# Performance work log

Measured on AMD Instinct MI355X. Metric: run time of the kernel, lower is better.

Reference implementation:

```python
import jax, jax.numpy as jnp
import numpy as np

B, S, H, NH, DH, F, L = 4, 2048, 512, 8, 64, 2048, 4
ALPHA = 1.0   # config.lag_time_scale_alpha
EPS = 1e-12   # BERT layer_norm_eps
MS_PER_MIN = 60.0 * 1000.0


def setup_inputs() -> dict:
    key = jax.random.key(0)
    ks = jax.random.split(key, 24)
    p = lambda k, shape: (jax.random.normal(k, shape, jnp.float32) * 0.02)
    inp = {
        "query_states": jax.random.normal(ks[0], (B, S, H), jnp.float32),
        "attention_mask": jnp.zeros((B, 1, 1, S), jnp.float32),
        "position_bias": jax.random.normal(ks[1], (1, NH, S, S), jnp.float32) * 0.02,
        "timestamp": jnp.sort(jax.random.randint(ks[2], (B, S), 0, 36_000_000, jnp.int32), axis=-1),
        # stacked per-layer parameters (L leading dim)
        "wq": p(ks[3], (L, H, H)), "bq": jnp.zeros((L, H), jnp.float32),
        "wk": p(ks[4], (L, H, H)), "bk": jnp.zeros((L, H), jnp.float32),
        "wv": p(ks[5], (L, H, H)), "bv": jnp.zeros((L, H), jnp.float32),
        "wo": p(ks[6], (L, H, H)), "bo": jnp.zeros((L, H), jnp.float32),
        "ln1_g": jnp.ones((L, H), jnp.float32), "ln1_b": jnp.zeros((L, H), jnp.float32),
        "wi": p(ks[7], (L, H, F)), "bi": jnp.zeros((L, F), jnp.float32),
        "wo2": p(ks[8], (L, F, H)), "bo2": jnp.zeros((L, H), jnp.float32),
        "ln2_g": jnp.ones((L, H), jnp.float32), "ln2_b": jnp.zeros((L, H), jnp.float32),
    }
    return inp


def _ln(x, g, b):
    m = x.mean(-1, keepdims=True)
    v = ((x - m) ** 2).mean(-1, keepdims=True)
    return (x - m) / jnp.sqrt(v + EPS) * g + b


def reference(query_states, attention_mask, position_bias, timestamp,
              wq, bq, wk, bk, wv, bv, wo, bo, ln1_g, ln1_b,
              wi, bi, wo2, bo2, ln2_g, ln2_b):
    # encoder (is_decoder=False) lag-time scale: (B,1,S,S)
    lag = (timestamp[:, None, :, None] - timestamp[:, None, None, :]).astype(jnp.float32) / MS_PER_MIN
    scale = np.sqrt(DH).astype(np.float32) - ALPHA / (jnp.clip(lag, 0.0) + 1.0) + ALPHA

    x = query_states
    for l in range(L):
        def proj(w, b):
            return (x @ w + b).reshape(B, S, NH, DH).transpose(0, 2, 1, 3)  # (B,NH,S,DH)
        q, k, v = proj(wq[l], bq[l]), proj(wk[l], bk[l]), proj(wv[l], bv[l])
        scores = jnp.einsum('bhqd,bhkd->bhqk', q, k) / scale + position_bias + attention_mask
        probs = jax.nn.softmax(scores, axis=-1)
        ctx = jnp.einsum('bhqk,bhkd->bhqd', probs, v).transpose(0, 2, 1, 3).reshape(B, S, H)
        attn = _ln(ctx @ wo[l] + bo[l] + x, ln1_g[l], ln1_b[l])
        ffn = jax.nn.gelu(attn @ wi[l] + bi[l], approximate=False) @ wo2[l] + bo2[l]
        x = _ln(ffn + attn, ln2_g[l], ln2_b[l])
    return x
```

## Files before the change

kernel.cpp:

```cpp
#include <hip/hip_runtime.h>
#include <stdint.h>

typedef unsigned short u16;
using half8   = __attribute__((ext_vector_type(8))) _Float16;
using half4v  = __attribute__((ext_vector_type(4))) _Float16;
using half2v  = __attribute__((ext_vector_type(2))) _Float16;
using float4v = __attribute__((ext_vector_type(4))) float;

#define L2E 1.4426950408889634f

__device__ inline float4v f4zero() { float4v z = {0.f, 0.f, 0.f, 0.f}; return z; }

__device__ inline u16 f2h(float f) {
  union { _Float16 h; u16 u; } v; v.h = (_Float16)f; return v.u;
}
__device__ inline float h2f(u16 u) {
  union { u16 u; _Float16 h; } v; v.u = u; return (float)v.h;
}

__device__ inline half2v cvtpk(float a, float b) {
  return __builtin_bit_cast(half2v, __builtin_amdgcn_cvt_pkrtz(a, b));
}
__device__ inline _Float16 hexp2_(_Float16 x) {
  _Float16 r;
  asm("v_exp_f16 %0, %1" : "=v"(r) : "v"(x));
  return r;
}
__device__ inline float fdot2f(half2v a, float c) {
#if __has_builtin(__builtin_amdgcn_fdot2)
  typedef __attribute__((ext_vector_type(2))) __fp16 h2r;
  return __builtin_amdgcn_fdot2(__builtin_bit_cast(h2r, a),
                                __builtin_bit_cast(h2r, 0x3C003C00u), c, false);
#else
  return c + (float)a.x + (float)a.y;
#endif
}

__device__ inline void glds16(const u16* g, u16* lds_base, int lane) {
#if __has_builtin(__builtin_amdgcn_global_load_lds)
  (void)lane;
  __builtin_amdgcn_global_load_lds((const __attribute__((address_space(1))) void*)g,
                                   (__attribute__((address_space(3))) void*)lds_base,
                                   16, 0, 0);
#else
  *(uint4*)(lds_base + (size_t)lane * 8) = *(const uint4*)g;
#endif
}

__global__ __launch_bounds__(256) void transpose_cast_kernel(
    const float* __restrict__ in, u16* __restrict__ out, int K, int N, size_t out_ls) {
  __shared__ float tile[32][33];
  const int tx = threadIdx.x & 31, ty = threadIdx.x >> 5;
  in  += (size_t)blockIdx.z * K * N;
  out += (size_t)blockIdx.z * out_ls;
  const int n  = blockIdx.x * 32 + tx;
  const int k0 = blockIdx.y * 32;
#pragma unroll
  for (int j = 0; j < 32; j += 8)
    tile[ty + j][tx] = in[(size_t)(k0 + ty + j) * N + n];
  __syncthreads();
  const int k = k0 + tx;
  const int n0 = blockIdx.x * 32;
#pragma unroll
  for (int j = 0; j < 32; j += 8)
    out[(size_t)(n0 + ty + j) * K + k] = f2h(tile[tx][ty + j]);
}

__global__ __launch_bounds__(256) void cast_kernel(const float* __restrict__ in,
                                                   u16* __restrict__ out) {
  const int i = (blockIdx.x * 256 + threadIdx.x) * 4;
  float4 t = *(const float4*)(in + i);
  ushort4 o;
  o.x = f2h(t.x); o.y = f2h(t.y); o.z = f2h(t.z); o.w = f2h(t.w);
  *(ushort4*)(out + i) = o;
}

__global__ __launch_bounds__(256) void pb_tile_kernel(const float* __restrict__ pb,
                                                      u16* __restrict__ pbT) {
  const int g  = blockIdx.x * 256 + threadIdx.x;
  const int mm = g & 15;
  const int q  = (g >> 4) & 2047;
  const int kbh = g >> 15;
  const int kb = kbh & 31, h = kbh >> 5;
  const float* src = pb + ((size_t)h * 2048 + q) * 2048 + kb * 64 + mm;
  ushort4 o;
  o.x = f2h(src[0]  * L2E);
  o.y = f2h(src[16] * L2E);
  o.z = f2h(src[32] * L2E);
  o.w = f2h(src[48] * L2E);
  *(ushort4*)(pbT + ((size_t)(h * 32 + kb) * 2048 + q) * 64 + mm * 4) = o;
}

__global__ __launch_bounds__(256) void inv_tile_kernel(const int* __restrict__ ts,
                                                       u16* __restrict__ invT) {
  const int g  = blockIdx.x * 256 + threadIdx.x;
  const int mm = g & 15;
  const int q  = (g >> 4) & 2047;
  const int kb = (g >> 15) & 31;
  const int b  = g >> 20;
  const int tq = ts[b * 2048 + q];
  ushort4 o;
  u16* op = (u16*)&o;
#pragma unroll
  for (int nb = 0; nb < 4; nb++) {
    const int k = kb * 64 + nb * 16 + mm;
    const int du = tq - ts[b * 2048 + k];
    const float u = (du > 0) ? (float)du : 0.f;
    op[nb] = f2h(fmaf(u, L2E, 86561.70245333781f) *
                 __builtin_amdgcn_rcpf(fmaf(u, 9.f, 480000.f)));
  }
  *(ushort4*)(invT + ((size_t)(b * 32 + kb) * 2048 + q) * 64 + mm * 4) = o;
}

__global__ __launch_bounds__(256) void maskts_kernel(const float* __restrict__ mask,
                                                     const int* __restrict__ ts,
                                                     float* __restrict__ maskE,
                                                     float* __restrict__ tsf) {
  const int i = blockIdx.x * 256 + threadIdx.x;
  maskE[i] = mask[i] * L2E;
  tsf[i]   = (float)ts[i];
}

template <int BM, int BN, int NN, int KK, int EPI>
__global__ __launch_bounds__(256) void gemm_kernel(
    const u16* __restrict__ A, const u16* __restrict__ Wt,
    const float* __restrict__ b0, const float* __restrict__ b1, const float* __restrict__ b2,
    const u16* __restrict__ resid,
    void* __restrict__ o0, void* __restrict__ o1, void* __restrict__ o2) {
  constexpr int FI = BM / 32;
  constexpr int FJB = BN / 32;
  constexpr int FIW = BM / 32;
  constexpr int FJW = BN / 32;
  constexpr int NT = KK / 64;
  __shared__ __align__(16) u16 smem[2 * BM * 64 + 2 * BN * 64];
  u16* As0 = smem;
  u16* Bs0 = smem + 2 * BM * 64;
  const int tid = threadIdx.x, lane = tid & 63, wv = tid >> 6;
  const int quad = lane >> 4, mm = lane & 15;
  const int m0 = blockIdx.x * BM, n0 = blockIdx.y * BN;
  const int wm = (wv >> 1) * (BM / 2), wn = (wv & 1) * (BN / 2);
  const int srow = tid >> 3, slot = tid & 7;
  const int chunk = slot ^ (srow & 7);
  const u16* Ag = A  + (size_t)(m0 + srow) * KK + chunk * 8;
  const u16* Bg = Wt + (size_t)(n0 + srow) * KK + chunk * 8;
  const int sw = mm & 7;

  float4v acc[FIW][FJW];
#pragma unroll
  for (int i = 0; i < FIW; i++)
#pragma unroll
    for (int j = 0; j < FJW; j++) acc[i][j] = f4zero();

#pragma unroll
  for (int i = 0; i < FI; i++)
    glds16(Ag + (size_t)i * 32 * KK, As0 + (size_t)(wv * 8 + i * 32) * 64, lane);
#pragma unroll
  for (int j = 0; j < FJB; j++)
    glds16(Bg + (size_t)j * 32 * KK, Bs0 + (size_t)(wv * 8 + j * 32) * 64, lane);

  int cur = 0;
#pragma unroll 2
  for (int kt = 0; kt < NT; kt++) {
    __syncthreads();

    if (kt + 1 < NT) {
      const size_t ko = (size_t)(kt + 1) * 64;
#pragma unroll
      for (int i = 0; i < FI; i++)
        glds16(Ag + (size_t)i * 32 * KK + ko,
               As0 + (size_t)(cur ^ 1) * BM * 64 + (size_t)(wv * 8 + i * 32) * 64, lane);
#pragma unroll
      for (int j = 0; j < FJB; j++)
        glds16(Bg + (size_t)j * 32 * KK + ko,
               Bs0 + (size_t)(cur ^ 1) * BN * 64 + (size_t)(wv * 8 + j * 32) * 64, lane);
    }

    const u16* Ac = As0 + (size_t)cur * BM * 64;
    const u16* Bc = Bs0 + (size_t)cur * BN * 64;
#pragma unroll
    for (int ks = 0; ks < 2; ks++) {
      half8 a[FIW], b[FJW];
#pragma unroll
      for (int i = 0; i < FIW; i++)
        a[i] = *(const half8*)(Ac + (size_t)(wm + i * 16 + mm) * 64 + (size_t)((ks * 4 + quad) ^ sw) * 8);
#pragma unroll
      for (int j = 0; j < FJW; j++)
        b[j] = *(const half8*)(Bc + (size_t)(wn + j * 16 + mm) * 64 + (size_t)((ks * 4 + quad) ^ sw) * 8);
#pragma unroll
      for (int i = 0; i < FIW; i++)
#pragma unroll
        for (int j = 0; j < FJW; j++)
          acc[i][j] = __builtin_amdgcn_mfma_f32_16x16x32_f16(a[i], b[j], acc[i][j], 0, 0, 0);
    }
    cur ^= 1;
  }

#pragma unroll
  for (int j = 0; j < FJW; j++) {
    const int gn = n0 + wn + j * 16 + mm;
    const float bias = b0[gn];
#pragma unroll
    for (int i = 0; i < FIW; i++)
#pragma unroll
      for (int r = 0; r < 4; r++) {
        const int gm = m0 + wm + i * 16 + quad * 4 + r;
        const float val = acc[i][j][r] + bias;
        const size_t idx = (size_t)gm * NN + gn;
        if (EPI == 2) {
          ((u16*)o0)[idx] = f2h(val);
        } else {
          const float z  = val * 0.70710678118654752f;
          const float az = fabsf(z);
          const float t  = __builtin_amdgcn_rcpf(1.0f + 0.3275911f * az);
          const float poly = t * (0.254829592f + t * (-0.284496736f +
                             t * (1.421413741f + t * (-1.453152027f + t * 1.061405429f))));
          const float e = __builtin_amdgcn_exp2f(-az * az * L2E);
          float erf_ = 1.0f - poly * e;
          erf_ = (z < 0.0f) ? -erf_ : erf_;
          ((u16*)o0)[idx] = f2h(val * 0.5f * (1.0f + erf_));
        }
      }
  }
  (void)b1; (void)b2; (void)o1; (void)o2; (void)resid;
}

template <int NN, int KK, int EPI>
__global__ __launch_bounds__(512) void gemm8_kernel(
    const u16* __restrict__ A, const u16* __restrict__ Wt,
    const float* __restrict__ b0, const float* __restrict__ b1, const float* __restrict__ b2,
    void* __restrict__ o0, void* __restrict__ o1, void* __restrict__ o2) {
  __shared__ __align__(16) u16 smem[256 * 64 + 128 * 64];
  u16* As = smem;
  u16* Bs = smem + 256 * 64;
  const int tid = threadIdx.x, lane = tid & 63, wv = tid >> 6;
  const int quad = lane >> 4, mm = lane & 15;
  const int m0 = blockIdx.x * 256, n0 = blockIdx.y * 128;
  const int wm = (wv >> 1) * 64, wn = (wv & 1) * 64;
  const int srow = tid >> 3, slot = tid & 7;
  const int chunk = slot ^ (srow & 7);
  const u16* Ag = A  + (size_t)(m0 + srow) * KK + chunk * 8;
  const u16* Bg = Wt + (size_t)(n0 + srow) * KK + chunk * 8;
  const int sw = mm & 7;

  float4v acc[4][4];
#pragma unroll
  for (int i = 0; i < 4; i++)
#pragma unroll
    for (int j = 0; j < 4; j++) acc[i][j] = f4zero();

  for (int kte = 0; kte < KK; kte += 64) {
#pragma unroll
    for (int p = 0; p < 4; p++)
      glds16(Ag + (size_t)(p * 64) * KK + kte, As + (size_t)(p * 64 + wv * 8) * 64, lane);
#pragma unroll
    for (int p = 0; p < 2; p++)
      glds16(Bg + (size_t)(p * 64) * KK + kte, Bs + (size_t)(p * 64 + wv * 8) * 64, lane);
    __syncthreads();

#pragma unroll
    for (int ks = 0; ks < 2; ks++) {
      half8 a[4], b[4];
#pragma unroll
      for (int i = 0; i < 4; i++)
        a[i] = *(const half8*)(As + (size_t)(wm + i * 16 + mm) * 64 + (size_t)((ks * 4 + quad) ^ sw) * 8);
#pragma unroll
      for (int j = 0; j < 4; j++)
        b[j] = *(const half8*)(Bs + (size_t)(wn + j * 16 + mm) * 64 + (size_t)((ks * 4 + quad) ^ sw) * 8);
#pragma unroll
      for (int i = 0; i < 4; i++)
#pragma unroll
        for (int j = 0; j < 4; j++)
          acc[i][j] = __builtin_amdgcn_mfma_f32_16x16x32_f16(a[i], b[j], acc[i][j], 0, 0, 0);
    }
    __syncthreads();
  }

  if constexpr (EPI == 4) {
    if (n0 >= 1024) {
      const int b_ = m0 >> 11, s_base = m0 & 2047;
      const int h0 = (n0 >> 6) & 7;
      u16* T = smem;
#pragma unroll
      for (int hp = 0; hp < 2; hp++) {
        __syncthreads();
        if ((wv >> 2) == hp) {
          const int lm = wm & 127;
#pragma unroll
          for (int j = 0; j < 4; j++) {
            const int cn = wn + j * 16 + mm;
            const float bias = b2[(n0 & 511) + cn];
#pragma unroll
            for (int i = 0; i < 4; i++)
#pragma unroll
              for (int r = 0; r < 4; r++)
                T[(lm + i * 16 + quad * 4 + r) * 130 + cn] = f2h(acc[i][j][r] + bias);
          }
        }
        __syncthreads();
        const int rr = tid >> 2, sq = tid & 3;
        const int hh = rr >> 6, dd = rr & 63;
        u16* outp = (u16*)o2 + ((size_t)((b_ * 8 + h0 + hh) * 64 + dd)) * 2048
                  + s_base + hp * 128 + sq * 32;
#pragma unroll
        for (int g = 0; g < 4; g++) {
          union { u16 u[8]; uint4 v; } pk;
#pragma unroll
          for (int e = 0; e < 8; e++) {
            const int sl = sq * 32 + g * 8 + e;
            const int tl = (sl & 64) + (((sl & 3) << 4) | ((sl & 63) >> 2));
            pk.u[e] = T[tl * 130 + rr];
          }
          *(uint4*)(outp + g * 8) = pk.v;
        }
      }
      return;
    }
#pragma unroll
    for (int j = 0; j < 4; j++) {
      const int gn = n0 + wn + j * 16 + mm;
      const int which = gn >> 9, col = gn & 511, h = (gn >> 6) & 7, d = gn & 63;
      const float* bp = (which == 0) ? b0 : b1;
      const float bias = bp[col];
      u16* dst = (which == 0) ? (u16*)o0 : (u16*)o1;
#pragma unroll
      for (int i = 0; i < 4; i++)
#pragma unroll
        for (int r = 0; r < 4; r++) {
          const int gm = m0 + wm + i * 16 + quad * 4 + r;
          const int b_ = gm >> 11, s_ = gm & 2047;
          dst[((size_t)((b_ * 8 + h) * 2048 + s_)) * 64 + d] = f2h(acc[i][j][r] + bias);
        }
    }
    return;
  }

#pragma unroll
  for (int j = 0; j < 4; j++) {
    const int gn = n0 + wn + j * 16 + mm;
    const float bias = b0[gn];
#pragma unroll
    for (int i = 0; i < 4; i++)
#pragma unroll
      for (int r = 0; r < 4; r++) {
        const int gm = m0 + wm + i * 16 + quad * 4 + r;
        const float val = acc[i][j][r] + bias;
        const size_t idx = (size_t)gm * NN + gn;
        const float z  = val * 0.70710678118654752f;
        const float az = fabsf(z);
        const float t  = __builtin_amdgcn_rcpf(1.0f + 0.3275911f * az);
        const float poly = t * (0.254829592f + t * (-0.284496736f +
                           t * (1.421413741f + t * (-1.453152027f + t * 1.061405429f))));
        const float e = __builtin_amdgcn_exp2f(-az * az * L2E);
        float erf_ = 1.0f - poly * e;
        erf_ = (z < 0.0f) ? -erf_ : erf_;
        ((u16*)o0)[idx] = f2h(val * 0.5f * (1.0f + erf_));
      }
  }
}

template <int TILED>
__global__ __launch_bounds__(512) void flash4_kernel(
    const u16* __restrict__ Q, const u16* __restrict__ Kb, const u16* __restrict__ Vt,
    const u16* __restrict__ pbT, const u16* __restrict__ invT,
    const float* __restrict__ pb32,
    const float* __restrict__ maskE, const float* __restrict__ tsf,
    u16* __restrict__ ctx) {
  __shared__ __align__(16) u16 Kls[2][64 * 64];
  __shared__ __align__(16) u16 Vls[2][64 * 64];
  __shared__ __align__(16) u16 P[8][16 * 64];
  const int tid = threadIdx.x, lane = tid & 63, w = tid >> 6;
  const int quad = lane >> 4, mm = lane & 15;
  const int bh = blockIdx.y, b_ = bh >> 3, h_ = bh & 7;
  const int q0 = blockIdx.x * 128 + w * 16;
  const size_t qk_base = (size_t)bh * 2048 * 64;
  const size_t v_base  = (size_t)bh * 64 * 2048;
  const int srow = lane >> 3, slot = lane & 7;
  const int chunk = slot ^ srow;
  const int sw = mm & 7;

  const u16* Kgl = Kb + qk_base + (size_t)(w * 8 + srow) * 64 + chunk * 8;
  const u16* Vgl = Vt + v_base + (size_t)(w * 8 + srow) * 2048 + chunk * 8;

  glds16(Kgl, &Kls[0][(w * 8) * 64], lane);
  glds16(Vgl, &Vls[0][(w * 8) * 64], lane);

  half8 aq[2];
#pragma unroll
  for (int t = 0; t < 2; t++)
    aq[t] = *(const half8*)(Q + qk_base + (size_t)(q0 + mm) * 64 + t * 32 + quad * 8);

  float tqf[4];
  if (TILED < 2) {
#pragma unroll
    for (int r = 0; r < 4; r++) tqf[r] = tsf[b_ * 2048 + q0 + quad * 4 + r];
  }

  float l_r[4] = {0.f, 0.f, 0.f, 0.f};
  float4v o[4];
#pragma unroll
  for (int ob = 0; ob < 4; ob++) o[ob] = f4zero();

  ushort4 pbc[4], invc[4]; float tkc[4], mkc[4];
  if (TILED >= 1) {
#pragma unroll
    for (int r = 0; r < 4; r++)
      pbc[r] = *(const ushort4*)(pbT + ((size_t)(h_ * 32) * 2048 + q0 + quad * 4 + r) * 64 + mm * 4);
  }
  if (TILED == 2) {
#pragma unroll
    for (int r = 0; r < 4; r++)
      invc[r] = *(const ushort4*)(invT + ((size_t)(b_ * 32) * 2048 + q0 + quad * 4 + r) * 64 + mm * 4);
  } else {
#pragma unroll
    for (int nb = 0; nb < 4; nb++) tkc[nb] = tsf[b_ * 2048 + nb * 16 + mm];
  }
#pragma unroll
  for (int nb = 0; nb < 4; nb++) mkc[nb] = maskE[b_ * 2048 + nb * 16 + mm];

  int cur = 0;
  for (int kt = 0; kt < 32; kt++) {
    const int k0 = kt * 64;
    __syncthreads();

    const int kn = (kt < 31) ? kt + 1 : kt;
    ushort4 pbn[4], invn[4]; float tkn[4], mkn[4];
    if (TILED >= 1) {
#pragma unroll
      for (int r = 0; r < 4; r++)
        pbn[r] = *(const ushort4*)(pbT + ((size_t)(h_ * 32 + kn) * 2048 + q0 + quad * 4 + r) * 64 + mm * 4);
    }
    if (TILED == 2) {
#pragma unroll
      for (int r = 0; r < 4; r++)
        invn[r] = *(const ushort4*)(invT + ((size_t)(b_ * 32 + kn) * 2048 + q0 + quad * 4 + r) * 64 + mm * 4);
    } else {
#pragma unroll
      for (int nb = 0; nb < 4; nb++) tkn[nb] = tsf[b_ * 2048 + kn * 64 + nb * 16 + mm];
    }
#pragma unroll
    for (int nb = 0; nb < 4; nb++) mkn[nb] = maskE[b_ * 2048 + kn * 64 + nb * 16 + mm];

    if (kt < 31) {
      const size_t ko = (size_t)(kt + 1) * 4096;
      const size_t vo = (size_t)(kt + 1) * 64;
      glds16(Kgl + ko, &Kls[cur ^ 1][(w * 8) * 64], lane);
      glds16(Vgl + vo, &Vls[cur ^ 1][(w * 8) * 64], lane);
    }

    const u16* Kc = Kls[cur];
    float4v s[4];
    __builtin_amdgcn_s_setprio(1);
#pragma unroll
    for (int nb = 0; nb < 4; nb++) {
      const half8 kf0 = *(const half8*)(Kc + (size_t)(nb * 16 + mm) * 64 + (size_t)(quad ^ sw) * 8);
      const half8 kf1 = *(const half8*)(Kc + (size_t)(nb * 16 + mm) * 64 + (size_t)((4 + quad) ^ sw) * 8);
      s[nb] = __builtin_amdgcn_mfma_f32_16x16x32_f16(aq[0], kf0, f4zero(), 0, 0, 0);
      s[nb] = __builtin_amdgcn_mfma_f32_16x16x32_f16(aq[1], kf1, s[nb], 0, 0, 0);
    }
    __builtin_amdgcn_s_setprio(0);

    const half2v mk01 = cvtpk(mkc[0], mkc[1]);
    const half2v mk23 = cvtpk(mkc[2], mkc[3]);
#pragma unroll
    for (int r = 0; r < 4; r++) {
      half2v pb01, pb23, iv01, iv23;
      if (TILED >= 1) {
        pb01 = *(const half2v*)&pbc[r].x;
        pb23 = *(const half2v*)&pbc[r].z;
      } else {
        float pv[4];
#pragma unroll
        for (int nb = 0; nb < 4; nb++)
          pv[nb] = pb32[((size_t)h_ * 2048 + q0 + quad * 4 + r) * 2048 + k0 + nb * 16 + mm] * L2E;
        pb01 = cvtpk(pv[0], pv[1]); pb23 = cvtpk(pv[2], pv[3]);
      }
      if (TILED == 2) {
        iv01 = *(const half2v*)&invc[r].x;
        iv23 = *(const half2v*)&invc[r].z;
      } else {
        float ivv[4];
#pragma unroll
        for (int nb = 0; nb < 4; nb++) {
          const float u = fmaxf(tqf[r] - tkc[nb], 0.f);
          ivv[nb] = fmaf(u, L2E, 86561.70245333781f) *
                    __builtin_amdgcn_rcpf(fmaf(u, 9.f, 480000.f));
        }
        iv01 = cvtpk(ivv[0], ivv[1]); iv23 = cvtpk(ivv[2], ivv[3]);
      }
      const half2v s01 = cvtpk(s[0][r], s[1][r]);
      const half2v s23 = cvtpk(s[2][r], s[3][r]);
      const half2v t01 = __builtin_elementwise_fma(s01, iv01, pb01 + mk01);
      const half2v t23 = __builtin_elementwise_fma(s23, iv23, pb23 + mk23);
      half2v p01, p23;
      p01.x = hexp2_(t01.x); p01.y = hexp2_(t01.y);
      p23.x = hexp2_(t23.x); p23.y = hexp2_(t23.y);
      l_r[r] = fdot2f(p01, l_r[r]);
      l_r[r] = fdot2f(p23, l_r[r]);
      const int prow = quad * 4 + r;
      union { half2v h2[2]; half4v h4; } uu;
      uu.h2[0] = p01; uu.h2[1] = p23;
      *(half4v*)((char*)P[w] + prow * 128 + ((mm * 8) ^ ((prow & 7) << 4))) = uu.h4;
    }

    const u16* Vc = Vls[cur];
    const char* Pb = (const char*)P[w] + mm * 128;
    const int pxor = (mm & 7) << 4;
    const half8 ap0 = *(const half8*)(Pb + ((quad * 16) ^ pxor));
    const half8 ap1 = *(const half8*)(Pb + ((64 + quad * 16) ^ pxor));
    __builtin_amdgcn_s_setprio(1);
#pragma unroll
    for (int ob = 0; ob < 4; ob++) {
      const half8 vf0 = *(const half8*)(Vc + (size_t)(ob * 16 + mm) * 64 + (size_t)(quad ^ sw) * 8);
      const half8 vf1 = *(const half8*)(Vc + (size_t)(ob * 16 + mm) * 64 + (size_t)((4 + quad) ^ sw) * 8);
      o[ob] = __builtin_amdgcn_mfma_f32_16x16x32_f16(ap0, vf0, o[ob], 0, 0, 0);
      o[ob] = __builtin_amdgcn_mfma_f32_16x16x32_f16(ap1, vf1, o[ob], 0, 0, 0);
    }
    __builtin_amdgcn_s_setprio(0);

#pragma unroll
    for (int r = 0; r < 4; r++) { pbc[r] = pbn[r]; invc[r] = invn[r]; }
#pragma unroll
    for (int nb = 0; nb < 4; nb++) { tkc[nb] = tkn[nb]; mkc[nb] = mkn[nb]; }
    cur ^= 1;
  }

#pragma unroll
  for (int r = 0; r < 4; r++) {
    float l = l_r[r];
#pragma unroll
    for (int sh = 1; sh < 16; sh <<= 1) l += __shfl_xor(l, sh, 64);
    const float rl = __builtin_amdgcn_rcpf(l);
    const int qrow = q0 + quad * 4 + r;
#pragma unroll
    for (int ob = 0; ob < 4; ob++)
      ctx[((size_t)b_ * 2048 + qrow) * 512 + h_ * 64 + ob * 16 + mm] = f2h(o[ob][r] * rl);
  }
}

__global__ __launch_bounds__(256) void ln_kernel(
    const u16* __restrict__ in, const u16* __restrict__ resid,
    const float* __restrict__ g, const float* __restrict__ bb,
    float* __restrict__ of, u16* __restrict__ obf) {
  const int lane = threadIdx.x & 63, w = threadIdx.x >> 6;
  const int row = blockIdx.x * 4 + w;
  const size_t base = (size_t)row * 512 + lane * 8;
  union { uint4 v; u16 u[8]; } a, b;
  a.v = *(const uint4*)(in + base);
  b.v = *(const uint4*)(resid + base);
  float v[8];
#pragma unroll
  for (int i = 0; i < 8; i++) v[i] = h2f(a.u[i]) + h2f(b.u[i]);
  float s = 0.f;
#pragma unroll
  for (int i = 0; i < 8; i++) s += v[i];
#pragma unroll
  for (int sh = 1; sh < 64; sh <<= 1) s += __shfl_xor(s, sh, 64);
  const float mean = s * (1.0f / 512.0f);
  float sq = 0.f;
#pragma unroll
  for (int i = 0; i < 8; i++) { const float d = v[i] - mean; sq += d * d; }
#pragma unroll
  for (int sh = 1; sh < 64; sh <<= 1) sq += __shfl_xor(sq, sh, 64);
  const float rstd = rsqrtf(sq * (1.0f / 512.0f) + 1e-12f);
#pragma unroll
  for (int i = 0; i < 8; i++) {
    const int col = lane * 8 + i;
    const float y = (v[i] - mean) * rstd * g[col] + bb[col];
    if (of) of[(size_t)row * 512 + col] = y;
    obf[(size_t)row * 512 + col] = f2h(y);
  }
}

extern "C" void kernel_launch(void* const* d_in, const int* in_sizes, int n_in,
                              void* d_out, int out_size, void* d_ws, size_t ws_size,
                              hipStream_t stream) {
  const float* x_in = (const float*)d_in[0];
  const float* mask = (const float*)d_in[1];
  const float* pb   = (const float*)d_in[2];
  const int*   ts   = (const int*)d_in[3];
  const float* wq = (const float*)d_in[4];  const float* bq = (const float*)d_in[5];
  const float* wk = (const float*)d_in[6];  const float* bk = (const float*)d_in[7];
  const float* wvp = (const float*)d_in[8]; const float* bv = (const float*)d_in[9];
  const float* wo = (const float*)d_in[10]; const float* bo = (const float*)d_in[11];
  const float* ln1g = (const float*)d_in[12]; const float* ln1b = (const float*)d_in[13];
  const float* wi = (const float*)d_in[14]; const float* bi = (const float*)d_in[15];
  const float* wo2 = (const float*)d_in[16]; const float* bo2 = (const float*)d_in[17];
  const float* ln2g = (const float*)d_in[18]; const float* ln2b = (const float*)d_in[19];

  char* ws = (char*)d_ws;
  const size_t o_wqkv  = 0;
  const size_t o_woT   = 6291456;
  const size_t o_wiT   = 8388608;
  const size_t o_wo2T  = 16777216;
  const size_t o_maskE = 25165824;
  const size_t o_tsf   = 25198592;
  const size_t o_xbf   = 25231360;
  const size_t o_qb    = 33619968;
  const size_t o_kb    = 42008576;
  const size_t o_vb    = 50397184;
  const size_t o_ctx   = 58785792;
  const size_t o_attnb = 67174400;
  const size_t o_tmp   = 75563008;
  const size_t o_pbT   = 92340224;
  const size_t o_invT  = 159449088;
  const int tiled = (ws_size >= o_invT + 33554432ull) ? 2
                  : (ws_size >= o_pbT + 67108864ull) ? 1 : 0;

  u16*   wqkvT = (u16*)(ws + o_wqkv);
  u16*   woT   = (u16*)(ws + o_woT);
  u16*   wiT   = (u16*)(ws + o_wiT);
  u16*   wo2T  = (u16*)(ws + o_wo2T);
  float* maskE = (float*)(ws + o_maskE);
  float* tsf   = (float*)(ws + o_tsf);
  u16*   xbf   = (u16*)(ws + o_xbf);
  u16*   qb    = (u16*)(ws + o_qb);
  u16*   kb    = (u16*)(ws + o_kb);
  u16*   vb    = (u16*)(ws + o_vb);
  u16*   ctx   = (u16*)(ws + o_ctx);
  u16*   hb    = (u16*)(ws + o_qb);
  u16*   attnb = (u16*)(ws + o_attnb);
  u16*   tmp16 = (u16*)(ws + o_tmp);
  u16*   pbT   = (u16*)(ws + o_pbT);
  u16*   invT  = (u16*)(ws + o_invT);

  const dim3 blk(256);
  const dim3 blk512(512);
  transpose_cast_kernel<<<dim3(16, 16, 4), blk, 0, stream>>>(wq,  wqkvT,          512, 512, 786432);
  transpose_cast_kernel<<<dim3(16, 16, 4), blk, 0, stream>>>(wk,  wqkvT + 262144, 512, 512, 786432);
  transpose_cast_kernel<<<dim3(16, 16, 4), blk, 0, stream>>>(wvp, wqkvT + 524288, 512, 512, 786432);
  transpose_cast_kernel<<<dim3(16, 16, 4), blk, 0, stream>>>(wo,  woT,  512, 512,  262144);
  transpose_cast_kernel<<<dim3(64, 16, 4), blk, 0, stream>>>(wi,  wiT,  512, 2048, 1048576);
  transpose_cast_kernel<<<dim3(16, 64, 4), blk, 0, stream>>>(wo2, wo2T, 2048, 512, 1048576);
  maskts_kernel<<<32, blk, 0, stream>>>(mask, ts, maskE, tsf);
  cast_kernel<<<4096, blk, 0, stream>>>(x_in, xbf);
  if (tiled >= 1) pb_tile_kernel<<<32768, blk, 0, stream>>>(pb, pbT);
  if (tiled == 2) inv_tile_kernel<<<16384, blk, 0, stream>>>(ts, invT);

  for (int l = 0; l < 4; l++) {
    gemm8_kernel<1536, 512, 4><<<dim3(32, 12), blk512, 0, stream>>>(
        xbf, wqkvT + (size_t)l * 786432, bq + l * 512, bk + l * 512, bv + l * 512,
        qb, kb, vb);
    if (tiled == 2)
      flash4_kernel<2><<<dim3(16, 32), blk512, 0, stream>>>(qb, kb, vb, pbT, invT, pb, maskE, tsf, ctx);
    else if (tiled == 1)
      flash4_kernel<1><<<dim3(16, 32), blk512, 0, stream>>>(qb, kb, vb, pbT, nullptr, pb, maskE, tsf, ctx);
    else
      flash4_kernel<0><<<dim3(16, 32), blk512, 0, stream>>>(qb, kb, vb, nullptr, nullptr, pb, maskE, tsf, ctx);
    gemm_kernel<128, 64, 512, 512, 2><<<dim3(64, 8), blk, 0, stream>>>(
        ctx, woT + (size_t)l * 262144, bo + l * 512, nullptr, nullptr, nullptr,
        tmp16, nullptr, nullptr);
    ln_kernel<<<2048, blk, 0, stream>>>(tmp16, xbf, ln1g + l * 512, ln1b + l * 512,
                                        nullptr, attnb);
    gemm8_kernel<2048, 512, 3><<<dim3(32, 16), blk512, 0, stream>>>(
        attnb, wiT + (size_t)l * 1048576, bi + l * 2048, nullptr, nullptr,
        hb, nullptr, nullptr);
    gemm_kernel<128, 64, 512, 2048, 2><<<dim3(64, 8), blk, 0, stream>>>(
        hb, wo2T + (size_t)l * 1048576, bo2 + l * 512, nullptr, nullptr, nullptr,
        tmp16, nullptr, nullptr);
    ln_kernel<<<2048, blk, 0, stream>>>(tmp16, attnb, ln2g + l * 512, ln2b + l * 512,
                                        (l == 3) ? (float*)d_out : nullptr, xbf);
  }
  (void)in_sizes; (void)n_in; (void)out_size;
}
```

Before: 1.125 ms.

## Split attention key range across two blocks and merge partial contexts

Adds a third grid dimension to the flash attention kernel so each block handles half of the key tiles. Each half writes a normalized fp16 partial context plus its row sum. A new combine kernel then merges the two halves, weighting each by its share of the total softmax denominator. The goal is to double the number of blocks and fill the GPU better, at the cost of extra partial-output traffic, another launch, and a second fp16 rounding step.

Result: slower. 1.161 ms (+3.2%).

```diff
diff --git a/kernel.cpp b/kernel.cpp
--- a/kernel.cpp
+++ b/kernel.cpp
@@ -364,13 +364,15 @@
     const u16* __restrict__ pbT, const u16* __restrict__ invT,
     const float* __restrict__ pb32,
     const float* __restrict__ maskE, const float* __restrict__ tsf,
-    u16* __restrict__ ctx) {
+    u16* __restrict__ ctxPart, float* __restrict__ lPart) {
   __shared__ __align__(16) u16 Kls[2][64 * 64];
   __shared__ __align__(16) u16 Vls[2][64 * 64];
   __shared__ __align__(16) u16 P[8][16 * 64];
   const int tid = threadIdx.x, lane = tid & 63, w = tid >> 6;
   const int quad = lane >> 4, mm = lane & 15;
   const int bh = blockIdx.y, b_ = bh >> 3, h_ = bh & 7;
+  const int z = blockIdx.z;
+  const int kt0 = z * 16, kt1 = kt0 + 16;
   const int q0 = blockIdx.x * 128 + w * 16;
   const size_t qk_base = (size_t)bh * 2048 * 64;
   const size_t v_base  = (size_t)bh * 64 * 2048;
@@ -381,8 +383,8 @@
   const u16* Kgl = Kb + qk_base + (size_t)(w * 8 + srow) * 64 + chunk * 8;
   const u16* Vgl = Vt + v_base + (size_t)(w * 8 + srow) * 2048 + chunk * 8;
 
-  glds16(Kgl, &Kls[0][(w * 8) * 64], lane);
-  glds16(Vgl, &Vls[0][(w * 8) * 64], lane);
+  glds16(Kgl + (size_t)kt0 * 4096, &Kls[0][(w * 8) * 64], lane);
+  glds16(Vgl + (size_t)kt0 * 64,   &Vls[0][(w * 8) * 64], lane);
 
   half8 aq[2];
 #pragma unroll
@@ -404,25 +406,25 @@
   if (TILED >= 1) {
 #pragma unroll
     for (int r = 0; r < 4; r++)
-      pbc[r] = *(const ushort4*)(pbT + ((size_t)(h_ * 32) * 2048 + q0 + quad * 4 + r) * 64 + mm * 4);
+      pbc[r] = *(const ushort4*)(pbT + ((size_t)(h_ * 32 + kt0) * 2048 + q0 + quad * 4 + r) * 64 + mm * 4);
   }
   if (TILED == 2) {
 #pragma unroll
     for (int r = 0; r < 4; r++)
-      invc[r] = *(const ushort4*)(invT + ((size_t)(b_ * 32) * 2048 + q0 + quad * 4 + r) * 64 + mm * 4);
+      invc[r] = *(const ushort4*)(invT + ((size_t)(b_ * 32 + kt0) * 2048 + q0 + quad * 4 + r) * 64 + mm * 4);
   } else {
 #pragma unroll
-    for (int nb = 0; nb < 4; nb++) tkc[nb] = tsf[b_ * 2048 + nb * 16 + mm];
-  }
-#pragma unroll
-  for (int nb = 0; nb < 4; nb++) mkc[nb] = maskE[b_ * 2048 + nb * 16 + mm];
+    for (int nb = 0; nb < 4; nb++) tkc[nb] = tsf[b_ * 2048 + kt0 * 64 + nb * 16 + mm];
+  }
+#pragma unroll
+  for (int nb = 0; nb < 4; nb++) mkc[nb] = maskE[b_ * 2048 + kt0 * 64 + nb * 16 + mm];
 
   int cur = 0;
-  for (int kt = 0; kt < 32; kt++) {
+  for (int kt = kt0; kt < kt1; kt++) {
     const int k0 = kt * 64;
     __syncthreads();
 
-    const int kn = (kt < 31) ? kt + 1 : kt;
+    const int kn = (kt < kt1 - 1) ? kt + 1 : kt;
     ushort4 pbn[4], invn[4]; float tkn[4], mkn[4];
     if (TILED >= 1) {
 #pragma unroll
@@ -440,11 +442,9 @@
 #pragma unroll
     for (int nb = 0; nb < 4; nb++) mkn[nb] = maskE[b_ * 2048 + kn * 64 + nb * 16 + mm];
 
-    if (kt < 31) {
-      const size_t ko = (size_t)(kt + 1) * 4096;
-      const size_t vo = (size_t)(kt + 1) * 64;
-      glds16(Kgl + ko, &Kls[cur ^ 1][(w * 8) * 64], lane);
-      glds16(Vgl + vo, &Vls[cur ^ 1][(w * 8) * 64], lane);
+    if (kt < kt1 - 1) {
+      glds16(Kgl + (size_t)(kt + 1) * 4096, &Kls[cur ^ 1][(w * 8) * 64], lane);
+      glds16(Vgl + (size_t)(kt + 1) * 64,   &Vls[cur ^ 1][(w * 8) * 64], lane);
     }
 
     const u16* Kc = Kls[cur];
@@ -524,6 +524,7 @@
     cur ^= 1;
   }
 
+  u16* cp = ctxPart + (size_t)z * (8192 * 512);
 #pragma unroll
   for (int r = 0; r < 4; r++) {
     float l = l_r[r];
@@ -533,8 +534,31 @@
     const int qrow = q0 + quad * 4 + r;
 #pragma unroll
     for (int ob = 0; ob < 4; ob++)
-      ctx[((size_t)b_ * 2048 + qrow) * 512 + h_ * 64 + ob * 16 + mm] = f2h(o[ob][r] * rl);
-  }
+      cp[((size_t)b_ * 2048 + qrow) * 512 + h_ * 64 + ob * 16 + mm] = f2h(o[ob][r] * rl);
+    if (mm == 0)
+      lPart[(size_t)z * 65536 + ((size_t)b_ * 2048 + qrow) * 8 + h_] = l;
+  }
+}
+
+__global__ __launch_bounds__(256) void combine_kernel(
+    const u16* __restrict__ cp, const float* __restrict__ lp,
+    u16* __restrict__ ctx) {
+  const int tid = threadIdx.x;
+  const int row = blockIdx.x * 4 + (tid >> 6);
+  const int lane = tid & 63;
+  const size_t idx = (size_t)row * 512 + lane * 8;
+  const int head = lane >> 3;
+  union { uint4 v; u16 u[8]; } a, b, o;
+  a.v = *(const uint4*)(cp + idx);
+  b.v = *(const uint4*)(cp + (size_t)8192 * 512 + idx);
+  const float l0 = lp[(size_t)row * 8 + head];
+  const float l1 = lp[65536 + (size_t)row * 8 + head];
+  const float rs = __builtin_amdgcn_rcpf(l0 + l1);
+  const float w0 = l0 * rs, w1 = l1 * rs;
+#pragma unroll
+  for (int i = 0; i < 8; i++)
+    o.u[i] = f2h(h2f(a.u[i]) * w0 + h2f(b.u[i]) * w1);
+  *(uint4*)(ctx + idx) = o.v;
 }
 
 __global__ __launch_bounds__(256) void ln_kernel(
@@ -620,6 +644,8 @@
   u16*   hb    = (u16*)(ws + o_qb);
   u16*   attnb = (u16*)(ws + o_attnb);
   u16*   tmp16 = (u16*)(ws + o_tmp);
+  u16*   ctxP  = (u16*)(ws + o_tmp);
+  float* lP    = (float*)(ws + o_attnb);
   u16*   pbT   = (u16*)(ws + o_pbT);
   u16*   invT  = (u16*)(ws + o_invT);
 
@@ -641,11 +667,12 @@
         xbf, wqkvT + (size_t)l * 786432, bq + l * 512, bk + l * 512, bv + l * 512,
         qb, kb, vb);
     if (tiled == 2)
-      flash4_kernel<2><<<dim3(16, 32), blk512, 0, stream>>>(qb, kb, vb, pbT, invT, pb, maskE, tsf, ctx);
+      flash4_kernel<2><<<dim3(16, 32, 2), blk512, 0, stream>>>(qb, kb, vb, pbT, invT, pb, maskE, tsf, ctxP, lP);
     else if (tiled == 1)
-      flash4_kernel<1><<<dim3(16, 32), blk512, 0, stream>>>(qb, kb, vb, pbT, nullptr, pb, maskE, tsf, ctx);
+      flash4_kernel<1><<<dim3(16, 32, 2), blk512, 0, stream>>>(qb, kb, vb, pbT, nullptr, pb, maskE, tsf, ctxP, lP);
     else
-      flash4_kernel<0><<<dim3(16, 32), blk512, 0, stream>>>(qb, kb, vb, nullptr, nullptr, pb, maskE, tsf, ctx);
+      flash4_kernel<0><<<dim3(16, 32, 2), blk512, 0, stream>>>(qb, kb, vb, nullptr, nullptr, pb, maskE, tsf, ctxP, lP);
+    combine_kernel<<<2048, blk, 0, stream>>>(ctxP, lP, ctx);
     gemm_kernel<128, 64, 512, 512, 2><<<dim3(64, 8), blk, 0, stream>>>(
         ctx, woT + (size_t)l * 262144, bo + l * 512, nullptr, nullptr, nullptr,
         tmp16, nullptr, nullptr);
```
